# Performance work log

Hardware: AMD Instinct MI355X
Metric: run time of the kernel (lower is better)

## Reference

```python
import jax, jax.numpy as jnp
import numpy as np

B, N, E, H = 8, 1500, 3000, 256
HOPS = 3


def setup_inputs() -> dict:
    key = jax.random.key(0)
    ks = jax.random.split(key, 9)
    node_state = jax.random.normal(ks[0], (B, N, H), jnp.float32)
    edge_vec = jax.random.normal(ks[1], (B, E, H), jnp.float32)
    # sparse-ish 0/1 incidence matrices (avg ~3 nonzeros per row)
    node2edge = (jax.random.uniform(ks[2], (B, E, N)) < 0.002).astype(jnp.float32)
    edge2node = (jax.random.uniform(ks[3], (B, N, E)) < 0.002).astype(jnp.float32)
    s = 1.0 / np.sqrt(H).astype(np.float32)
    W_max = jax.random.uniform(ks[4], (H, H), jnp.float32, -s, s)        # linear_max, no bias
    W_fz = jax.random.uniform(ks[5], (4 * H, H), jnp.float32, -s, s)     # gated fusion
    b_fz = jnp.zeros((H,), jnp.float32)
    W_z = jax.random.uniform(ks[6], (2 * H, H), jnp.float32, -s, s)      # GRU gates, no bias
    W_r = jax.random.uniform(ks[7], (2 * H, H), jnp.float32, -s, s)
    W_t = jax.random.uniform(ks[8], (2 * H, H), jnp.float32, -s, s)
    return dict(node_state=node_state, edge_vec=edge_vec, node2edge=node2edge,
                edge2node=edge2node, W_max=W_max, W_fz=W_fz, b_fz=b_fz,
                W_z=W_z, W_r=W_r, W_t=W_t)


def _msg_pass(node_state, edge_vec, n2e, e2n):
    # n2e: (B,E,N), e2n: (B,N,E)
    edge_emb = jnp.einsum('ben,bnh->beh', n2e, node_state) + edge_vec   # (B,E,H)
    norm = jnp.sum(e2n, axis=2, keepdims=True) + 1.0                     # self-loop degree norm
    return (jnp.einsum('bne,beh->bnh', e2n, edge_emb) + node_state) / norm


def _gated_fusion(h, x, W_fz, b_fz):
    z = jax.nn.sigmoid(jnp.concatenate([h, x, h * x, h - x], -1) @ W_fz + b_fz)
    return (1.0 - z) * h + z * x


def _gru_step(h, x, W_z, W_r, W_t):
    hx = jnp.concatenate([h, x], -1)
    z = jax.nn.sigmoid(hx @ W_z)
    r = jax.nn.sigmoid(hx @ W_r)
    t = jnp.tanh(jnp.concatenate([r * h, x], -1) @ W_t)
    return (1.0 - z) * h + z * t


def reference(node_state, edge_vec, node2edge, edge2node, W_max, W_fz, b_fz, W_z, W_r, W_t):
    n2e_T = jnp.swapaxes(node2edge, 1, 2)   # (B,N,E)
    e2n_T = jnp.swapaxes(edge2node, 1, 2)   # (B,E,N)
    for _ in range(HOPS):
        bw = _msg_pass(node_state, edge_vec, node2edge, edge2node)
        fw = _msg_pass(node_state, edge_vec, e2n_T, n2e_T)
        agg = _gated_fusion(fw, bw, W_fz, b_fz)
        node_state = _gru_step(node_state, agg, W_z, W_r, W_t)
    # graph max pool: linear then max over nodes
    graph_embedding = jnp.max(node_state @ W_max, axis=1)[None]  # (1,B,H)
    return jnp.swapaxes(node_state, 0, 1), graph_embedding       # (N,B,H), (1,B,H)
```

## Files before the change

### kernel.cpp

```cpp
#include <hip/hip_runtime.h>
#include <hip/hip_bf16.h>
#include <stdint.h>

#define Bb 8
#define Nn 1500
#define Ee 3000
#define Hh 256
#define NHOPS 3
#define CAP 32
#define Mrows (Bb*Nn)
#define BE (Bb*Ee)
#define BN (Bb*Nn)
#define TOTQ 9000000

typedef __bf16 bf16x8 __attribute__((ext_vector_type(8)));
typedef float f32x4 __attribute__((ext_vector_type(4)));

__device__ __forceinline__ float sigmoidf_(float x){ return 1.f/(1.f+__expf(-x)); }

__device__ __forceinline__ unsigned short f2b(float f){
  union { float f; unsigned int u; } x; x.f = f;
  unsigned int r = (x.u + 0x7fffu + ((x.u >> 16) & 1u)) >> 16;
  return (unsigned short)r;
}
__device__ __forceinline__ float b2f(unsigned short u){
  union { unsigned int u; float f; } x; x.u = ((unsigned int)u) << 16;
  return x.f;
}
__device__ __forceinline__ ushort4 pack4(float4 v){
  return make_ushort4(f2b(v.x), f2b(v.y), f2b(v.z), f2b(v.w));
}
__device__ __forceinline__ float4 unpack4(ushort4 u){
  return make_float4(b2f(u.x), b2f(u.y), b2f(u.z), b2f(u.w));
}
__device__ __forceinline__ unsigned fkey(float f){
  unsigned u = __float_as_uint(f);
  return (u & 0x80000000u) ? ~u : (u | 0x80000000u);
}

#define GLL16(g, l) __builtin_amdgcn_global_load_lds( \
    (const __attribute__((address_space(1))) unsigned int*)(g), \
    (__attribute__((address_space(3))) unsigned int*)(l), 16, 0, 0)

__device__ __forceinline__ void scan_proc(float4 vv, int t,
    int* __restrict__ Aidx, int* __restrict__ cntA, int* __restrict__ Didx, int* __restrict__ cntD,
    int* __restrict__ Bidx, int* __restrict__ cntB, int* __restrict__ Cidx, int* __restrict__ cntC) {
  if (vv.x == 0.f && vv.y == 0.f && vv.z == 0.f && vv.w == 0.f) return;
  int *rowIdx, *rowCnt, *colIdx, *colCnt;
  int g, q, R, C;
  if (t < TOTQ) {
    rowIdx = Aidx; rowCnt = cntA; colIdx = Didx; colCnt = cntD;
    R = Ee; C = Nn;
    g = t / 375; q = t - g * 375;
  } else {
    int tt = t - TOTQ;
    rowIdx = Bidx; rowCnt = cntB; colIdx = Cidx; colCnt = cntC;
    R = Nn; C = Ee;
    g = tt / 750; q = tt - g * 750;
  }
  int b = g / R;
  int r = g - b * R;
  int cbase = q * 4;
  #pragma unroll
  for (int j = 0; j < 4; ++j) {
    float vj = (j == 0) ? vv.x : (j == 1) ? vv.y : (j == 2) ? vv.z : vv.w;
    if (vj != 0.f) {
      int c = cbase + j;
      int rs = atomicAdd(&rowCnt[g], 1);
      if (rs < CAP) rowIdx[(size_t)g * CAP + rs] = c;
      int cs = atomicAdd(&colCnt[b * C + c], 1);
      if (cs < CAP) colIdx[(size_t)(b * C + c) * CAP + cs] = r;
    }
  }
}

__global__ void scan_kernel(const float4* __restrict__ n2e4, const float4* __restrict__ e2n4,
                            int* __restrict__ Aidx, int* __restrict__ cntA,
                            int* __restrict__ Didx, int* __restrict__ cntD,
                            int* __restrict__ Bidx, int* __restrict__ cntB,
                            int* __restrict__ Cidx, int* __restrict__ cntC) {
  int t0 = blockIdx.x * 1024 + threadIdx.x;
  float4 v[4];
  int ts[4];
  #pragma unroll
  for (int r2 = 0; r2 < 4; ++r2) {
    int t = t0 + r2 * 256;
    ts[r2] = t;
    const float4* p = (t < TOTQ) ? (n2e4 + t) : (e2n4 + (t - TOTQ));
    v[r2] = (t < 2 * TOTQ) ? *p : make_float4(0.f, 0.f, 0.f, 0.f);
  }
  __builtin_amdgcn_sched_barrier(0);
  #pragma unroll
  for (int r2 = 0; r2 < 4; ++r2)
    scan_proc(v[r2], ts[r2], Aidx, cntA, Didx, cntD, Bidx, cntB, Cidx, cntC);
}

__global__ void prep_kernel(const float* __restrict__ Wfz, const float* __restrict__ Wz,
                            const float* __restrict__ Wr, const float* __restrict__ Wt,
                            const float* __restrict__ Wmax,
                            unsigned short* __restrict__ WfzT, unsigned short* __restrict__ WzrT,
                            unsigned short* __restrict__ WtT, unsigned short* __restrict__ WmaxT,
                            const float* __restrict__ in_ns, unsigned short* __restrict__ nsb,
                            const float* __restrict__ in_ev, unsigned short* __restrict__ evb) {
  int bx = blockIdx.x;
  if (bx < 2560) {
    int t = bx * 256 + threadIdx.x;
    if (t < 196608) {
      int n = t / 768, k = t % 768;
      float v;
      if (k < 256)      v = Wfz[k * 256 + n] + Wfz[(k + 768) * 256 + n];
      else if (k < 512) v = Wfz[k * 256 + n] - Wfz[(k + 512) * 256 + n];
      else              v = Wfz[k * 256 + n];
      WfzT[t] = f2b(v);
    } else if (t < 458752) {
      int u = t - 196608;
      int j = u >> 9, k = u & 511;
      float v = (j < 256) ? Wz[k * 256 + j] : Wr[k * 256 + (j - 256)];
      WzrT[u] = f2b(v);
    } else if (t < 589824) {
      int u = t - 458752;
      int n = u >> 9, k = u & 511;
      WtT[u] = f2b(Wt[k * 256 + n]);
    } else if (t < 655360) {
      int u = t - 589824;
      int n = u >> 8, k = u & 255;
      WmaxT[u] = f2b(Wmax[k * 256 + n]);
    }
  } else if (bx < 3310) {
    int t0 = (bx - 2560) * 1024 + threadIdx.x;
    #pragma unroll
    for (int r = 0; r < 4; ++r) {
      int t = t0 + r * 256;
      ((ushort4*)nsb)[t] = pack4(((const float4*)in_ns)[t]);
    }
  } else {
    int t0 = (bx - 3310) * 1024 + threadIdx.x;
    #pragma unroll
    for (int r = 0; r < 4; ++r) {
      int t = t0 + r * 256;
      ((ushort4*)evb)[t] = pack4(((const float4*)in_ev)[t]);
    }
  }
}

__device__ __forceinline__ void sort_one(int* pp, int c) {
  if (c > CAP) c = CAP;
  int v[CAP];
  for (int j = 0; j < c; ++j) v[j] = pp[j];
  for (int j = 1; j < c; ++j) { int key = v[j]; int k = j - 1;
    while (k >= 0 && v[k] > key) { v[k+1] = v[k]; --k; } v[k+1] = key; }
  for (int j = 0; j < c; ++j) pp[j] = v[j];
}
__global__ void sort4_kernel(int* __restrict__ Cidx, const int* __restrict__ cntC,
                             int* __restrict__ Didx, const int* __restrict__ cntD,
                             int* __restrict__ Aidx, const int* __restrict__ cntA,
                             int* __restrict__ Bidx, const int* __restrict__ cntB) {
  int i = blockIdx.x * 256 + threadIdx.x;
  if (i < BE) sort_one(Cidx + (size_t)i * CAP, cntC[i]);
  else if (i < BE + BN) { int k = i - BE; sort_one(Didx + (size_t)k * CAP, cntD[k]); }
  else if (i < 2 * BE + BN) { int k = i - BE - BN; sort_one(Aidx + (size_t)k * CAP, cntA[k]); }
  else if (i < 2 * BE + 2 * BN) { int k = i - 2 * BE - BN; sort_one(Bidx + (size_t)k * CAP, cntB[k]); }
}

__global__ void edge_kernel(const ushort4* __restrict__ evb4, const ushort4* __restrict__ nsb4,
                            const int* __restrict__ Aidx, const int* __restrict__ Acnt,
                            const int* __restrict__ Cidx, const int* __restrict__ Ccnt,
                            ushort4* __restrict__ eb4, ushort4* __restrict__ ef4) {
  int w = __builtin_amdgcn_readfirstlane((int)(threadIdx.x >> 6));
  int be = blockIdx.x * 4 + w;
  int lane = threadIdx.x & 63;
  int b = be / Ee;
  int cA = min(Acnt[be], CAP), cC = min(Ccnt[be], CAP);
  const int* pA = Aidx + (size_t)be * CAP;
  const int* pC = Cidx + (size_t)be * CAP;
  float4 ev = unpack4(evb4[(size_t)be * 64 + lane]);
  float4 sA = ev, sC = ev;
  for (int i = 0; i < cA; ++i) {
    int n = pA[i];
    float4 t = unpack4(nsb4[((size_t)b * Nn + n) * 64 + lane]);
    sA.x += t.x; sA.y += t.y; sA.z += t.z; sA.w += t.w;
  }
  for (int i = 0; i < cC; ++i) {
    int n = pC[i];
    float4 t = unpack4(nsb4[((size_t)b * Nn + n) * 64 + lane]);
    sC.x += t.x; sC.y += t.y; sC.z += t.z; sC.w += t.w;
  }
  eb4[(size_t)be * 64 + lane] = pack4(sA);
  ef4[(size_t)be * 64 + lane] = pack4(sC);
}

__global__ void node_kernel(const float4* __restrict__ nsin4,
                            const ushort4* __restrict__ eb4, const ushort4* __restrict__ ef4,
                            const int* __restrict__ Bidx, const int* __restrict__ Bcnt,
                            const int* __restrict__ Didx, const int* __restrict__ Dcnt,
                            ushort4* __restrict__ Xfz4, ushort4* __restrict__ Xzr4) {
  int w = __builtin_amdgcn_readfirstlane((int)(threadIdx.x >> 6));
  int bn = blockIdx.x * 4 + w;
  int lane = threadIdx.x & 63;
  int b = bn / Nn;
  int rB = Bcnt[bn], rD = Dcnt[bn];
  int cB = min(rB, CAP), cD = min(rD, CAP);
  const int* pB = Bidx + (size_t)bn * CAP;
  const int* pD = Didx + (size_t)bn * CAP;
  float4 h0 = nsin4[(size_t)bn * 64 + lane];
  float4 sb = h0, sf = h0;
  for (int i = 0; i < cB; ++i) {
    int e = pB[i];
    float4 t = unpack4(eb4[((size_t)b * Ee + e) * 64 + lane]);
    sb.x += t.x; sb.y += t.y; sb.z += t.z; sb.w += t.w;
  }
  for (int i = 0; i < cD; ++i) {
    int e = pD[i];
    float4 t = unpack4(ef4[((size_t)b * Ee + e) * 64 + lane]);
    sf.x += t.x; sf.y += t.y; sf.z += t.z; sf.w += t.w;
  }
  float ib = 1.f / (1.f + (float)rB), idf = 1.f / (1.f + (float)rD);
  sb.x *= ib; sb.y *= ib; sb.z *= ib; sb.w *= ib;
  sf.x *= idf; sf.y *= idf; sf.z *= idf; sf.w *= idf;
  float4 prod = make_float4(sf.x*sb.x, sf.y*sb.y, sf.z*sb.z, sf.w*sb.w);
  size_t m = bn;
  Xfz4[m * 192 +   0 + lane] = pack4(sf);
  Xfz4[m * 192 +  64 + lane] = pack4(sb);
  Xfz4[m * 192 + 128 + lane] = pack4(prod);
  Xzr4[m * 128 + lane] = pack4(h0);
}

#define EPI_FZ   1
#define EPI_ZR   2
#define EPI_GRU  3
#define EPI_MAX  4

template<int EPI, int LAST>
__global__ __launch_bounds__(512) void gemm_kernel(
    const unsigned short* __restrict__ A, const unsigned short* __restrict__ WT,
    int M, int K,
    unsigned* __restrict__ gkey, const float* __restrict__ bfz,
    unsigned short* __restrict__ Xzr, unsigned short* __restrict__ zbuf,
    unsigned short* __restrict__ Xt,
    const float* __restrict__ nsin, float* __restrict__ nsout,
    unsigned short* __restrict__ nsbout)
{
  __shared__ unsigned short As[128 * 64];
  __shared__ unsigned short Bs[64 * 64];
  int m0 = blockIdx.x * 128, n0 = blockIdx.y * 64;
  int tid = threadIdx.x;
  int lane = tid & 63;
  int wid = __builtin_amdgcn_readfirstlane(tid >> 6);
  int wm = wid >> 1, wn = wid & 1;
  int p = lane >> 4;
  int q = lane & 7;
  int lr = lane >> 3;
  f32x4 acc[2][2] = {};
  for (int k0 = 0; k0 < K; k0 += 64) {
    {
      int rl0 = wid * 16 + lr;
      int gm0 = m0 + rl0; if (gm0 > M - 1) gm0 = M - 1;
      GLL16(A + (size_t)gm0 * K + k0 + ((q ^ (rl0 & 7)) << 3), &As[(wid * 16) * 64]);
      int rl1 = rl0 + 8;
      int gm1 = m0 + rl1; if (gm1 > M - 1) gm1 = M - 1;
      GLL16(A + (size_t)gm1 * K + k0 + ((q ^ (rl1 & 7)) << 3), &As[(wid * 16 + 8) * 64]);
      int rb = wid * 8 + lr;
      GLL16(WT + (size_t)(n0 + rb) * K + k0 + ((q ^ (rb & 7)) << 3), &Bs[(wid * 8) * 64]);
    }
    __syncthreads();
    #pragma unroll
    for (int kk = 0; kk < 64; kk += 32) {
      int cq = (kk >> 3) + p;
      int ra0 = wm * 32 + (lane & 15);
      int ra1 = ra0 + 16;
      int rb0 = wn * 32 + (lane & 15);
      int rb1 = rb0 + 16;
      bf16x8 a0 = *(const bf16x8*)&As[ra0 * 64 + ((cq ^ (ra0 & 7)) << 3)];
      bf16x8 a1 = *(const bf16x8*)&As[ra1 * 64 + ((cq ^ (ra1 & 7)) << 3)];
      bf16x8 b0 = *(const bf16x8*)&Bs[rb0 * 64 + ((cq ^ (rb0 & 7)) << 3)];
      bf16x8 b1 = *(const bf16x8*)&Bs[rb1 * 64 + ((cq ^ (rb1 & 7)) << 3)];
      acc[0][0] = __builtin_amdgcn_mfma_f32_16x16x32_bf16(a0, b0, acc[0][0], 0, 0, 0);
      acc[0][1] = __builtin_amdgcn_mfma_f32_16x16x32_bf16(a0, b1, acc[0][1], 0, 0, 0);
      acc[1][0] = __builtin_amdgcn_mfma_f32_16x16x32_bf16(a1, b0, acc[1][0], 0, 0, 0);
      acc[1][1] = __builtin_amdgcn_mfma_f32_16x16x32_bf16(a1, b1, acc[1][1], 0, 0, 0);
    }
    __syncthreads();
  }
  if (EPI == EPI_MAX) {
    #pragma unroll
    for (int mi = 0; mi < 2; ++mi)
    #pragma unroll
    for (int ni = 0; ni < 2; ++ni) {
      int mb = m0 + wm * 32 + mi * 16 + p * 4;
      int c = n0 + wn * 32 + ni * 16 + (lane & 15);
      if (mb >= M) continue;
      int b0 = mb / Nn, b3 = (mb + 3) / Nn;
      if (b0 == b3) {
        float mx = fmaxf(fmaxf(acc[mi][ni][0], acc[mi][ni][1]),
                         fmaxf(acc[mi][ni][2], acc[mi][ni][3]));
        atomicMax(&gkey[b0 * 256 + c], fkey(mx));
      } else {
        #pragma unroll
        for (int j = 0; j < 4; ++j)
          atomicMax(&gkey[((mb + j) / Nn) * 256 + c], fkey(acc[mi][ni][j]));
      }
    }
    return;
  }
  #pragma unroll
  for (int mi = 0; mi < 2; ++mi)
  #pragma unroll
  for (int ni = 0; ni < 2; ++ni)
  #pragma unroll
  for (int j = 0; j < 4; ++j) {
    int m = m0 + wm * 32 + mi * 16 + p * 4 + j;
    int c = n0 + wn * 32 + ni * 16 + (lane & 15);
    if (m >= M) continue;
    float v = acc[mi][ni][j];
    if (EPI == EPI_FZ) {
      float z = sigmoidf_(v + bfz[c]);
      float fw = b2f(A[(size_t)m * K + c]);
      float bw = b2f(A[(size_t)m * K + 256 + c]);
      unsigned short agg = f2b((1.f - z) * fw + z * bw);
      Xzr[(size_t)m * 512 + 256 + c] = agg;
      Xt[(size_t)m * 512 + 256 + c] = agg;
    } else if (EPI == EPI_ZR) {
      float s = sigmoidf_(v);
      if (c < 256) {
        zbuf[(size_t)m * 256 + c] = f2b(s);
      } else {
        int cz = c - 256;
        Xt[(size_t)m * 512 + cz] = f2b(s * nsin[(size_t)m * 256 + cz]);
      }
    } else {
      float t = tanhf(v);
      float zz = b2f(zbuf[(size_t)m * 256 + c]);
      float h = nsin[(size_t)m * 256 + c];
      float nh = (1.f - zz) * h + zz * t;
      nsbout[(size_t)m * 256 + c] = f2b(nh);
      if (LAST) {
        int bb = m / Nn, n = m - bb * Nn;
        nsout[((size_t)n * Bb + bb) * 256 + c] = nh;
      } else {
        nsout[(size_t)m * 256 + c] = nh;
      }
    }
  }
}

__global__ void maxfin_kernel(const unsigned* __restrict__ gkey, float* __restrict__ out) {
  int t = blockIdx.x * 256 + threadIdx.x;
  if (t >= Bb * Hh) return;
  unsigned k = gkey[t];
  unsigned u = (k & 0x80000000u) ? (k & 0x7fffffffu) : ~k;
  out[(size_t)Nn * Bb * Hh + t] = __uint_as_float(u);
}

extern "C" void kernel_launch(void* const* d_in, const int* in_sizes, int n_in,
                              void* d_out, int out_size, void* d_ws, size_t ws_size,
                              hipStream_t stream) {
  const float* in_ns   = (const float*)d_in[0];
  const float* in_ev   = (const float*)d_in[1];
  const float* in_n2e  = (const float*)d_in[2];
  const float* in_e2n  = (const float*)d_in[3];
  const float* in_wmax = (const float*)d_in[4];
  const float* in_wfz  = (const float*)d_in[5];
  const float* in_bfz  = (const float*)d_in[6];
  const float* in_wz   = (const float*)d_in[7];
  const float* in_wr   = (const float*)d_in[8];
  const float* in_wt   = (const float*)d_in[9];
  float* out = (float*)d_out;

  char* base = (char*)d_ws;
  size_t off = 0;
  auto alloc = [&](size_t bytes) -> void* {
    void* r = base + off;
    off = (off + bytes + 255) & ~(size_t)255;
    return r;
  };
  int* cnts = (int*)alloc((size_t)(2 * BE + 2 * BN) * 4);
  unsigned* gkey = (unsigned*)alloc(Bb * Hh * 4);
  int* cntC = cnts;
  int* cntD = cnts + BE;
  int* cntA = cnts + BE + BN;
  int* cntB = cnts + BE + BN + BE;
  int* Aidx = (int*)alloc((size_t)BE * CAP * 4);
  int* Bidx = (int*)alloc((size_t)BN * CAP * 4);
  int* Cidx = (int*)alloc((size_t)BE * CAP * 4);
  int* Didx = (int*)alloc((size_t)BN * CAP * 4);
  float* ns   = (float*)alloc((size_t)Mrows * Hh * 4);
  unsigned short* nsb = (unsigned short*)alloc((size_t)Mrows * Hh * 2);
  unsigned short* evb = (unsigned short*)alloc((size_t)BE * Hh * 2);
  unsigned short* eb = (unsigned short*)alloc((size_t)BE * Hh * 2);
  unsigned short* ef = (unsigned short*)alloc((size_t)BE * Hh * 2);
  unsigned short* Xfz = (unsigned short*)alloc((size_t)Mrows * 768 * 2);
  unsigned short* Xzr = (unsigned short*)alloc((size_t)Mrows * 512 * 2);
  unsigned short* Xt  = (unsigned short*)alloc((size_t)Mrows * 512 * 2);
  unsigned short* zbuf = (unsigned short*)alloc((size_t)Mrows * 256 * 2);
  unsigned short* WfzT  = (unsigned short*)alloc(256 * 768 * 2);
  unsigned short* WzrT  = (unsigned short*)alloc(512 * 512 * 2);
  unsigned short* WtT   = (unsigned short*)alloc(256 * 512 * 2);
  unsigned short* WmaxT = (unsigned short*)alloc(256 * 256 * 2);
  (void)ws_size; (void)in_sizes; (void)n_in; (void)out_size;

  hipMemsetAsync(cnts, 0, (size_t)(2 * BE + 2 * BN) * 4 + (size_t)Bb * Hh * 4, stream);

  scan_kernel<<<(2 * TOTQ + 1023) / 1024, 256, 0, stream>>>(
      (const float4*)in_n2e, (const float4*)in_e2n,
      Aidx, cntA, Didx, cntD, Bidx, cntB, Cidx, cntC);
  prep_kernel<<<4810, 256, 0, stream>>>(
      in_wfz, in_wz, in_wr, in_wt, in_wmax,
      WfzT, WzrT, WtT, WmaxT,
      in_ns, nsb, in_ev, evb);
  sort4_kernel<<<(2 * BE + 2 * BN + 255) / 256, 256, 0, stream>>>(
      Cidx, cntC, Didx, cntD, Aidx, cntA, Bidx, cntB);

  dim3 gFZ(94, 4), gZR(94, 8), gT(94, 4);
  for (int hop = 0; hop < NHOPS; ++hop) {
    const float* nsin = (hop == 0) ? in_ns : ns;
    edge_kernel<<<BE / 4, 256, 0, stream>>>((const ushort4*)evb, (const ushort4*)nsb,
        Aidx, cntA, Cidx, cntC, (ushort4*)eb, (ushort4*)ef);
    node_kernel<<<BN / 4, 256, 0, stream>>>((const float4*)nsin,
        (const ushort4*)eb, (const ushort4*)ef,
        Bidx, cntB, Didx, cntD, (ushort4*)Xfz, (ushort4*)Xzr);
    gemm_kernel<EPI_FZ, 0><<<gFZ, 512, 0, stream>>>(Xfz, WfzT, Mrows, 768,
        nullptr, in_bfz, Xzr, nullptr, Xt, nullptr, nullptr, nullptr);
    gemm_kernel<EPI_ZR, 0><<<gZR, 512, 0, stream>>>(Xzr, WzrT, Mrows, 512,
        nullptr, nullptr, nullptr, zbuf, Xt, nsin, nullptr, nullptr);
    if (hop < NHOPS - 1) {
      gemm_kernel<EPI_GRU, 0><<<gT, 512, 0, stream>>>(Xt, WtT, Mrows, 512,
          nullptr, nullptr, nullptr, zbuf, nullptr, nsin, ns, nsb);
    } else {
      gemm_kernel<EPI_GRU, 1><<<gT, 512, 0, stream>>>(Xt, WtT, Mrows, 512,
          nullptr, nullptr, nullptr, zbuf, nullptr, nsin, out, nsb);
    }
  }

  gemm_kernel<EPI_MAX, 0><<<gT, 512, 0, stream>>>(nsb, WmaxT, Mrows, 256,
      gkey, nullptr, nullptr, nullptr, nullptr, nullptr, nullptr, nullptr);
  maxfin_kernel<<<(Bb * Hh + 255) / 256, 256, 0, stream>>>(gkey, out);
}
```

Measured before the change: 443.1 us.

## Precompose incidence into node-to-node lists and hoist hop-invariant edge-vector aggregation

Replaces the per-hop two-stage gather (nodes to edges, then edges to nodes) with one node-level gather over precomputed node-to-node index lists, built once from the composed incidence structure. The edge_vec contribution, which does not change across hops, is aggregated once per direction into per-node buffers before the hop loop. This removes the per-hop edge kernel and its intermediate edge buffers. Node features in the node kernel now come from the bf16 copy instead of fp32, and the scan kernel handles 8 chunks per thread instead of 4. The cost is extra setup kernels and index storage, lists capped at 128 entries, and slightly different rounding since edge sums are no longer stored in bf16.

```diff
diff --git a/kernel.cpp b/kernel.cpp
--- a/kernel.cpp
+++ b/kernel.cpp
@@ -8,6 +8,7 @@
 #define Hh 256
 #define NHOPS 3
 #define CAP 32
+#define MCAP 128
 #define Mrows (Bb*Nn)
 #define BE (Bb*Ee)
 #define BN (Bb*Nn)
@@ -79,11 +80,11 @@
                             int* __restrict__ Didx, int* __restrict__ cntD,
                             int* __restrict__ Bidx, int* __restrict__ cntB,
                             int* __restrict__ Cidx, int* __restrict__ cntC) {
-  int t0 = blockIdx.x * 1024 + threadIdx.x;
-  float4 v[4];
-  int ts[4];
-  #pragma unroll
-  for (int r2 = 0; r2 < 4; ++r2) {
+  int t0 = blockIdx.x * 2048 + threadIdx.x;
+  float4 v[8];
+  int ts[8];
+  #pragma unroll
+  for (int r2 = 0; r2 < 8; ++r2) {
     int t = t0 + r2 * 256;
     ts[r2] = t;
     const float4* p = (t < TOTQ) ? (n2e4 + t) : (e2n4 + (t - TOTQ));
@@ -91,7 +92,7 @@
   }
   __builtin_amdgcn_sched_barrier(0);
   #pragma unroll
-  for (int r2 = 0; r2 < 4; ++r2)
+  for (int r2 = 0; r2 < 8; ++r2)
     scan_proc(v[r2], ts[r2], Aidx, cntA, Didx, cntD, Bidx, cntB, Cidx, cntC);
 }
 
@@ -100,8 +101,7 @@
                             const float* __restrict__ Wmax,
                             unsigned short* __restrict__ WfzT, unsigned short* __restrict__ WzrT,
                             unsigned short* __restrict__ WtT, unsigned short* __restrict__ WmaxT,
-                            const float* __restrict__ in_ns, unsigned short* __restrict__ nsb,
-                            const float* __restrict__ in_ev, unsigned short* __restrict__ evb) {
+                            const float* __restrict__ in_ns, unsigned short* __restrict__ nsb) {
   int bx = blockIdx.x;
   if (bx < 2560) {
     int t = bx * 256 + threadIdx.x;
@@ -126,19 +126,12 @@
       int n = u >> 8, k = u & 255;
       WmaxT[u] = f2b(Wmax[k * 256 + n]);
     }
-  } else if (bx < 3310) {
+  } else {
     int t0 = (bx - 2560) * 1024 + threadIdx.x;
     #pragma unroll
     for (int r = 0; r < 4; ++r) {
       int t = t0 + r * 256;
       ((ushort4*)nsb)[t] = pack4(((const float4*)in_ns)[t]);
-    }
-  } else {
-    int t0 = (bx - 3310) * 1024 + threadIdx.x;
-    #pragma unroll
-    for (int r = 0; r < 4; ++r) {
-      int t = t0 + r * 256;
-      ((ushort4*)evb)[t] = pack4(((const float4*)in_ev)[t]);
     }
   }
 }
@@ -162,59 +155,95 @@
   else if (i < 2 * BE + 2 * BN) { int k = i - 2 * BE - BN; sort_one(Bidx + (size_t)k * CAP, cntB[k]); }
 }
 
-__global__ void edge_kernel(const ushort4* __restrict__ evb4, const ushort4* __restrict__ nsb4,
-                            const int* __restrict__ Aidx, const int* __restrict__ Acnt,
-                            const int* __restrict__ Cidx, const int* __restrict__ Ccnt,
-                            ushort4* __restrict__ eb4, ushort4* __restrict__ ef4) {
+__global__ void mbuild_kernel(const int* __restrict__ Bidx, const int* __restrict__ cntB,
+                              const int* __restrict__ Aidx, const int* __restrict__ cntA,
+                              const int* __restrict__ Didx, const int* __restrict__ cntD,
+                              const int* __restrict__ Cidx, const int* __restrict__ cntC,
+                              int* __restrict__ M1idx, int* __restrict__ m1cnt,
+                              int* __restrict__ M2idx, int* __restrict__ m2cnt) {
+  int t = blockIdx.x * 256 + threadIdx.x;
+  if (t < BN) {
+    int i = t, b = i / Nn;
+    int ec = min(cntB[i], CAP);
+    const int* pe = Bidx + (size_t)i * CAP;
+    int mc = 0;
+    int* dst = M1idx + (size_t)i * MCAP;
+    for (int k = 0; k < ec; ++k) {
+      int be = b * Ee + pe[k];
+      int na = min(cntA[be], CAP);
+      const int* pn = Aidx + (size_t)be * CAP;
+      for (int u = 0; u < na && mc < MCAP; ++u) dst[mc++] = pn[u];
+    }
+    m1cnt[i] = mc;
+  } else if (t < 2 * BN) {
+    int i = t - BN, b = i / Nn;
+    int ec = min(cntD[i], CAP);
+    const int* pe = Didx + (size_t)i * CAP;
+    int mc = 0;
+    int* dst = M2idx + (size_t)i * MCAP;
+    for (int k = 0; k < ec; ++k) {
+      int be = b * Ee + pe[k];
+      int na = min(cntC[be], CAP);
+      const int* pn = Cidx + (size_t)be * CAP;
+      for (int u = 0; u < na && mc < MCAP; ++u) dst[mc++] = pn[u];
+    }
+    m2cnt[i] = mc;
+  }
+}
+
+__global__ void evagg_kernel(const float4* __restrict__ ev4,
+                             const int* __restrict__ Bidx, const int* __restrict__ cntB,
+                             const int* __restrict__ Didx, const int* __restrict__ cntD,
+                             ushort4* __restrict__ eva1, ushort4* __restrict__ eva2) {
+  int bx = blockIdx.x;
   int w = __builtin_amdgcn_readfirstlane((int)(threadIdx.x >> 6));
-  int be = blockIdx.x * 4 + w;
   int lane = threadIdx.x & 63;
-  int b = be / Ee;
-  int cA = min(Acnt[be], CAP), cC = min(Ccnt[be], CAP);
-  const int* pA = Aidx + (size_t)be * CAP;
-  const int* pC = Cidx + (size_t)be * CAP;
-  float4 ev = unpack4(evb4[(size_t)be * 64 + lane]);
-  float4 sA = ev, sC = ev;
-  for (int i = 0; i < cA; ++i) {
-    int n = pA[i];
-    float4 t = unpack4(nsb4[((size_t)b * Nn + n) * 64 + lane]);
-    sA.x += t.x; sA.y += t.y; sA.z += t.z; sA.w += t.w;
-  }
-  for (int i = 0; i < cC; ++i) {
-    int n = pC[i];
-    float4 t = unpack4(nsb4[((size_t)b * Nn + n) * 64 + lane]);
-    sC.x += t.x; sC.y += t.y; sC.z += t.z; sC.w += t.w;
-  }
-  eb4[(size_t)be * 64 + lane] = pack4(sA);
-  ef4[(size_t)be * 64 + lane] = pack4(sC);
-}
-
-__global__ void node_kernel(const float4* __restrict__ nsin4,
-                            const ushort4* __restrict__ eb4, const ushort4* __restrict__ ef4,
-                            const int* __restrict__ Bidx, const int* __restrict__ Bcnt,
-                            const int* __restrict__ Didx, const int* __restrict__ Dcnt,
+  int dir = bx >= 3000;
+  int i = (dir ? bx - 3000 : bx) * 4 + w;
+  int b = i / Nn;
+  const int* pe = (dir ? Didx : Bidx) + (size_t)i * CAP;
+  int ec = min((dir ? cntD : cntB)[i], CAP);
+  float4 s = make_float4(0.f, 0.f, 0.f, 0.f);
+  for (int k = 0; k < ec; ++k) {
+    int e = pe[k];
+    float4 t = ev4[((size_t)b * Ee + e) * 64 + lane];
+    s.x += t.x; s.y += t.y; s.z += t.z; s.w += t.w;
+  }
+  (dir ? eva2 : eva1)[(size_t)i * 64 + lane] = pack4(s);
+}
+
+__global__ void node_kernel(const ushort4* __restrict__ nsb4,
+                            const ushort4* __restrict__ eva1, const ushort4* __restrict__ eva2,
+                            const int* __restrict__ M1idx, const int* __restrict__ m1cnt,
+                            const int* __restrict__ M2idx, const int* __restrict__ m2cnt,
+                            const int* __restrict__ cntB, const int* __restrict__ cntD,
                             ushort4* __restrict__ Xfz4, ushort4* __restrict__ Xzr4) {
   int w = __builtin_amdgcn_readfirstlane((int)(threadIdx.x >> 6));
   int bn = blockIdx.x * 4 + w;
   int lane = threadIdx.x & 63;
   int b = bn / Nn;
-  int rB = Bcnt[bn], rD = Dcnt[bn];
-  int cB = min(rB, CAP), cD = min(rD, CAP);
-  const int* pB = Bidx + (size_t)bn * CAP;
-  const int* pD = Didx + (size_t)bn * CAP;
-  float4 h0 = nsin4[(size_t)bn * 64 + lane];
-  float4 sb = h0, sf = h0;
-  for (int i = 0; i < cB; ++i) {
-    int e = pB[i];
-    float4 t = unpack4(eb4[((size_t)b * Ee + e) * 64 + lane]);
+  size_t nbase = (size_t)b * Nn;
+  ushort4 h0u = nsb4[(size_t)bn * 64 + lane];
+  float4 h0 = unpack4(h0u);
+  float4 sb = unpack4(eva1[(size_t)bn * 64 + lane]);
+  sb.x += h0.x; sb.y += h0.y; sb.z += h0.z; sb.w += h0.w;
+  int c1 = m1cnt[bn];
+  const int* p1 = M1idx + (size_t)bn * MCAP;
+  for (int k = 0; k < c1; ++k) {
+    int j = p1[k];
+    float4 t = unpack4(nsb4[(nbase + j) * 64 + lane]);
     sb.x += t.x; sb.y += t.y; sb.z += t.z; sb.w += t.w;
   }
-  for (int i = 0; i < cD; ++i) {
-    int e = pD[i];
-    float4 t = unpack4(ef4[((size_t)b * Ee + e) * 64 + lane]);
+  float4 sf = unpack4(eva2[(size_t)bn * 64 + lane]);
+  sf.x += h0.x; sf.y += h0.y; sf.z += h0.z; sf.w += h0.w;
+  int c2 = m2cnt[bn];
+  const int* p2 = M2idx + (size_t)bn * MCAP;
+  for (int k = 0; k < c2; ++k) {
+    int j = p2[k];
+    float4 t = unpack4(nsb4[(nbase + j) * 64 + lane]);
     sf.x += t.x; sf.y += t.y; sf.z += t.z; sf.w += t.w;
   }
-  float ib = 1.f / (1.f + (float)rB), idf = 1.f / (1.f + (float)rD);
+  float ib = 1.f / (1.f + (float)cntB[bn]), idf = 1.f / (1.f + (float)cntD[bn]);
   sb.x *= ib; sb.y *= ib; sb.z *= ib; sb.w *= ib;
   sf.x *= idf; sf.y *= idf; sf.z *= idf; sf.w *= idf;
   float4 prod = make_float4(sf.x*sb.x, sf.y*sb.y, sf.z*sb.z, sf.w*sb.w);
@@ -222,7 +251,7 @@
   Xfz4[m * 192 +   0 + lane] = pack4(sf);
   Xfz4[m * 192 +  64 + lane] = pack4(sb);
   Xfz4[m * 192 + 128 + lane] = pack4(prod);
-  Xzr4[m * 128 + lane] = pack4(h0);
+  Xzr4[m * 128 + lane] = h0u;
 }
 
 #define EPI_FZ   1
@@ -383,11 +412,14 @@
   int* Bidx = (int*)alloc((size_t)BN * CAP * 4);
   int* Cidx = (int*)alloc((size_t)BE * CAP * 4);
   int* Didx = (int*)alloc((size_t)BN * CAP * 4);
+  int* M1idx = (int*)alloc((size_t)BN * MCAP * 4);
+  int* M2idx = (int*)alloc((size_t)BN * MCAP * 4);
+  int* m1cnt = (int*)alloc(BN * 4);
+  int* m2cnt = (int*)alloc(BN * 4);
   float* ns   = (float*)alloc((size_t)Mrows * Hh * 4);
   unsigned short* nsb = (unsigned short*)alloc((size_t)Mrows * Hh * 2);
-  unsigned short* evb = (unsigned short*)alloc((size_t)BE * Hh * 2);
-  unsigned short* eb = (unsigned short*)alloc((size_t)BE * Hh * 2);
-  unsigned short* ef = (unsigned short*)alloc((size_t)BE * Hh * 2);
+  unsigned short* eva1 = (unsigned short*)alloc((size_t)BN * Hh * 2);
+  unsigned short* eva2 = (unsigned short*)alloc((size_t)BN * Hh * 2);
   unsigned short* Xfz = (unsigned short*)alloc((size_t)Mrows * 768 * 2);
   unsigned short* Xzr = (unsigned short*)alloc((size_t)Mrows * 512 * 2);
   unsigned short* Xt  = (unsigned short*)alloc((size_t)Mrows * 512 * 2);
@@ -400,24 +432,28 @@
 
   hipMemsetAsync(cnts, 0, (size_t)(2 * BE + 2 * BN) * 4 + (size_t)Bb * Hh * 4, stream);
 
-  scan_kernel<<<(2 * TOTQ + 1023) / 1024, 256, 0, stream>>>(
+  scan_kernel<<<(2 * TOTQ + 2047) / 2048, 256, 0, stream>>>(
       (const float4*)in_n2e, (const float4*)in_e2n,
       Aidx, cntA, Didx, cntD, Bidx, cntB, Cidx, cntC);
-  prep_kernel<<<4810, 256, 0, stream>>>(
+  prep_kernel<<<3310, 256, 0, stream>>>(
       in_wfz, in_wz, in_wr, in_wt, in_wmax,
-      WfzT, WzrT, WtT, WmaxT,
-      in_ns, nsb, in_ev, evb);
+      WfzT, WzrT, WtT, WmaxT, in_ns, nsb);
   sort4_kernel<<<(2 * BE + 2 * BN + 255) / 256, 256, 0, stream>>>(
       Cidx, cntC, Didx, cntD, Aidx, cntA, Bidx, cntB);
+  mbuild_kernel<<<(2 * BN + 255) / 256, 256, 0, stream>>>(
+      Bidx, cntB, Aidx, cntA, Didx, cntD, Cidx, cntC,
+      M1idx, m1cnt, M2idx, m2cnt);
+  evagg_kernel<<<6000, 256, 0, stream>>>(
+      (const float4*)in_ev, Bidx, cntB, Didx, cntD,
+      (ushort4*)eva1, (ushort4*)eva2);
 
   dim3 gFZ(94, 4), gZR(94, 8), gT(94, 4);
   for (int hop = 0; hop < NHOPS; ++hop) {
     const float* nsin = (hop == 0) ? in_ns : ns;
-    edge_kernel<<<BE / 4, 256, 0, stream>>>((const ushort4*)evb, (const ushort4*)nsb,
-        Aidx, cntA, Cidx, cntC, (ushort4*)eb, (ushort4*)ef);
-    node_kernel<<<BN / 4, 256, 0, stream>>>((const float4*)nsin,
-        (const ushort4*)eb, (const ushort4*)ef,
-        Bidx, cntB, Didx, cntD, (ushort4*)Xfz, (ushort4*)Xzr);
+    node_kernel<<<BN / 4, 256, 0, stream>>>((const ushort4*)nsb,
+        (const ushort4*)eva1, (const ushort4*)eva2,
+        M1idx, m1cnt, M2idx, m2cnt, cntB, cntD,
+        (ushort4*)Xfz, (ushort4*)Xzr);
     gemm_kernel<EPI_FZ, 0><<<gFZ, 512, 0, stream>>>(Xfz, WfzT, Mrows, 768,
         nullptr, in_bfz, Xzr, nullptr, Xt, nullptr, nullptr, nullptr);
     gemm_kernel<EPI_ZR, 0><<<gZR, 512, 0, stream>>>(Xzr, WzrT, Mrows, 512,
```

Result: slower. 503.8 us (+13.7%).
